# Performance work log

Measured on AMD Instinct MI355X. Metric: run time of the kernel, lower is better.

Reference implementation:

```python
import jax, jax.numpy as jnp
import numpy as np

NUM_UNITS = 512
NUM_IN = 256
BATCH = 8192


def _to_complex(x):
    # torch.view_as_complex on x.view(B, N, 2): even cols real, odd cols imag
    x2 = x.reshape(x.shape[0], -1, 2)
    return jax.lax.complex(x2[..., 0], x2[..., 1])


def _diag_mul(w, z):
    return (jnp.cos(w) + 1j * jnp.sin(w)) * z


def _reflect(re, im, z):
    v = jax.lax.complex(re, im)                      # [N]
    vstar_z = jnp.sum(jnp.conj(v) * z, axis=1, keepdims=True)  # [B,1]
    sq_norm = jnp.sum(re * re + im * im)
    return z - (2.0 / sq_norm) * vstar_z * v


def _modrelu(z, bias):
    norm = jnp.abs(z)
    scale = jax.nn.relu(norm + bias) / (norm + 1e-6)
    return scale * z


def setup_inputs() -> dict:
    key = jax.random.key(0)
    ks = jax.random.split(key, 12)
    two_pi = 2.0 * np.pi
    inputs = jax.random.normal(ks[0], (BATCH, NUM_IN), dtype=jnp.float32)
    states = jax.random.normal(ks[1], (BATCH, 2 * NUM_UNITS), dtype=jnp.float32)
    # xavier_uniform for w_ih [2N, num_in]
    bound = np.sqrt(6.0 / (2 * NUM_UNITS + NUM_IN)).astype(np.float32)
    w_ih = jax.random.uniform(ks[2], (2 * NUM_UNITS, NUM_IN), jnp.float32, -bound, bound)
    b_h = jnp.zeros((NUM_UNITS,), jnp.float32)
    d1_w = jax.random.uniform(ks[3], (NUM_UNITS,), jnp.float32, -np.pi, np.pi)
    d2_w = jax.random.uniform(ks[4], (NUM_UNITS,), jnp.float32, -np.pi, np.pi)
    d3_w = jax.random.uniform(ks[5], (NUM_UNITS,), jnp.float32, -np.pi, np.pi)
    r1_re = jax.random.uniform(ks[6], (NUM_UNITS,), jnp.float32, -1.0, 1.0)
    r1_im = jax.random.uniform(ks[7], (NUM_UNITS,), jnp.float32, -1.0, 1.0)
    r2_re = jax.random.uniform(ks[8], (NUM_UNITS,), jnp.float32, -1.0, 1.0)
    r2_im = jax.random.uniform(ks[9], (NUM_UNITS,), jnp.float32, -1.0, 1.0)
    perm = jax.random.permutation(ks[10], NUM_UNITS).astype(jnp.int64)
    return {"inputs": inputs, "states": states, "w_ih": w_ih, "b_h": b_h,
            "d1_w": d1_w, "r1_re": r1_re, "r1_im": r1_im, "perm": perm,
            "d2_w": d2_w, "r2_re": r2_re, "r2_im": r2_im, "d3_w": d3_w}


def reference(inputs, states, w_ih, b_h, d1_w, r1_re, r1_im, perm,
              d2_w, r2_re, r2_im, d3_w):
    inputs_mul = inputs @ w_ih.T                      # [B, 2N]
    inputs_mul_c = _to_complex(inputs_mul)            # [B, N] complex
    state_c = _to_complex(states)                     # [B, N] complex

    z = _diag_mul(d1_w, state_c)
    z = jnp.fft.fft(z, axis=1)
    z = _reflect(r1_re, r1_im, z)
    z = z[:, perm]
    z = _diag_mul(d2_w, z)
    z = jnp.fft.ifft(z, axis=1)
    z = _reflect(r2_re, r2_im, z)
    z = _diag_mul(d3_w, z)

    preact = inputs_mul_c + z
    new_c = _modrelu(preact, b_h)
    return jnp.concatenate([new_c.real, new_c.imag], axis=1)  # [B, 2N]
```

## Files before the change

kernel.cpp:

```cpp
#include <hip/hip_runtime.h>
#include <math.h>

#define BATCH 8192
#define NU 512
#define NIN 256

typedef __attribute__((ext_vector_type(8))) __bf16 bf16x8;
typedef __attribute__((ext_vector_type(4))) float f32x4;

__device__ __forceinline__ float2 cmul(float2 a, float2 b){
    return make_float2(a.x*b.x - a.y*b.y, a.x*b.y + a.y*b.x);
}
__device__ __forceinline__ float2 cadd(float2 a, float2 b){ return make_float2(a.x+b.x, a.y+b.y); }
__device__ __forceinline__ float2 csub(float2 a, float2 b){ return make_float2(a.x-b.x, a.y-b.y); }

__device__ __forceinline__ float2 cis_native(float ang){
    return make_float2(__cosf(ang), __sinf(ang));
}

template<bool INV>
__device__ __forceinline__ float2 twid512(int idx){
    float ang = 0.012271846303085129f * (float)idx;
    return cis_native(INV ? ang : -ang);
}

__device__ __forceinline__ unsigned int pack2bf(float x, float y){
    unsigned int ux = __float_as_uint(x);
    ux = (ux + 0x7FFFu + ((ux >> 16) & 1u)) >> 16;
    unsigned int uy = __float_as_uint(y);
    uy = (uy + 0x7FFFu + ((uy >> 16) & 1u)) & 0xFFFF0000u;
    return ux | uy;
}


__device__ __forceinline__ void stage_tile(const float* __restrict__ G,
                                           char* __restrict__ lds,
                                           int kb, int tid){
    const int r0 = tid >> 3;
    const int kc = (tid & 7) << 3;
    #pragma unroll
    for (int it = 0; it < 4; ++it){
        const int row = r0 + (it << 5);
        const float* g = G + (size_t)row * NIN + kb + kc;
        float4 v0 = *(const float4*)g;
        float4 v1 = *(const float4*)(g + 4);
        int4 w;
        w.x = (int)pack2bf(v0.x, v0.y);
        w.y = (int)pack2bf(v0.z, v0.w);
        w.z = (int)pack2bf(v1.x, v1.y);
        w.w = (int)pack2bf(v1.z, v1.w);
        int off = (row << 7) + (kc << 1);
        off ^= (row & 7) << 4;
        *(int4*)(lds + off) = w;
    }
}

__global__ __launch_bounds__(256) void gemm_bf16(const float* __restrict__ A,
                                                 const float* __restrict__ W,
                                                 float* __restrict__ P){
    __shared__ __align__(16) char smem[2 * 128*64*2];
    char* As = smem;
    char* Bs = smem + 128*64*2;
    const int tid  = threadIdx.x;
    const int lane = tid & 63, wv = tid >> 6;
    const int wm = wv >> 1, wn = wv & 1;
    const int bm = blockIdx.y, bn = blockIdx.x;

    const float* Ag = A + (size_t)bm * 128 * NIN;
    const float* Wg = W + (size_t)bn * 128 * NIN;

    f32x4 acc[4][4] = {};
    const int frow = lane & 15;
    const int kq   = (lane >> 4) << 4;

    for (int kb = 0; kb < NIN; kb += 64){
        if (kb) __syncthreads();
        stage_tile(Ag, As, kb, tid);
        stage_tile(Wg, Bs, kb, tid);
        __syncthreads();
        #pragma unroll
        for (int ks = 0; ks < 2; ++ks){
            const int koff = kq + (ks << 6);
            bf16x8 a[4], b[4];
            #pragma unroll
            for (int i = 0; i < 4; ++i){
                const int ar = wm*64 + i*16 + frow;
                a[i] = *(const bf16x8*)(As + (((ar << 7) + koff) ^ ((ar & 7) << 4)));
                const int br = wn*64 + i*16 + frow;
                b[i] = *(const bf16x8*)(Bs + (((br << 7) + koff) ^ ((br & 7) << 4)));
            }
            #pragma unroll
            for (int mi = 0; mi < 4; ++mi)
                #pragma unroll
                for (int ni = 0; ni < 4; ++ni)
                    acc[mi][ni] = __builtin_amdgcn_mfma_f32_16x16x32_bf16(
                        a[mi], b[ni], acc[mi][ni], 0, 0, 0);
        }
    }

    float* stg = (float*)smem;
    const int lr4 = (lane >> 4) << 2;
    #pragma unroll
    for (int q = 0; q < 4; ++q){
        __syncthreads();
        if (wm == (q >> 1)){
            const int miBase = (q & 1) * 2;
            #pragma unroll
            for (int mj = 0; mj < 2; ++mj)
                #pragma unroll
                for (int ni = 0; ni < 4; ++ni)
                    #pragma unroll
                    for (int r = 0; r < 4; ++r)
                        stg[(lr4 + mj*16 + r)*132 + wn*64 + ni*16 + frow]
                            = acc[miBase + mj][ni][r];
        }
        __syncthreads();
        #pragma unroll
        for (int it = 0; it < 4; ++it){
            int idx = it*256 + tid;
            int r32 = idx >> 5;
            int c4  = idx & 31;
            float4 v = *(const float4*)(stg + r32*132 + c4*4);
            int grow = bm*128 + (q >> 1)*64 + (q & 1)*32 + r32;
            *(float4*)(P + (size_t)grow*1024 + bn*128 + c4*4) = v;
        }
    }
}


__device__ __forceinline__ void fft_fwd(float2 z[8], int l){
    #pragma unroll
    for (int r = 0; r < 4; ++r){
        float2 w = twid512<false>(r*64 + l);
        float2 a = z[r], b = z[r+4];
        z[r]   = cadd(a, b);
        z[r+4] = cmul(w, csub(a, b));
    }
    {
        float2 w0 = twid512<false>(2*l), w1 = twid512<false>(2*(64+l));
        const int gs[4] = {0,1,4,5};
        #pragma unroll
        for (int k = 0; k < 4; ++k){
            int g = gs[k];
            float2 w = (g & 1) ? w1 : w0;
            float2 a = z[g], b = z[g+2];
            z[g]   = cadd(a, b);
            z[g+2] = cmul(w, csub(a, b));
        }
    }
    {
        float2 w = twid512<false>(4*l);
        #pragma unroll
        for (int g = 0; g < 8; g += 2){
            float2 a = z[g], b = z[g+1];
            z[g]   = cadd(a, b);
            z[g+1] = cmul(w, csub(a, b));
        }
    }
    #pragma unroll
    for (int h = 32; h >= 1; h >>= 1){
        int m = 256 / h;
        float2 w = twid512<false>(m * (l & (h-1)));
        bool low = (l & h) != 0;
        #pragma unroll
        for (int r = 0; r < 8; ++r){
            float2 p;
            p.x = __shfl_xor(z[r].x, h);
            p.y = __shfl_xor(z[r].y, h);
            z[r] = low ? cmul(w, csub(p, z[r])) : cadd(z[r], p);
        }
    }
}

__device__ __forceinline__ void fft_inv(float2 z[8], int l){
    #pragma unroll
    for (int h = 1; h <= 32; h <<= 1){
        int m = 256 / h;
        float2 w = twid512<true>(m * (l & (h-1)));
        bool low = (l & h) != 0;
        #pragma unroll
        for (int r = 0; r < 8; ++r){
            float2 p;
            p.x = __shfl_xor(z[r].x, h);
            p.y = __shfl_xor(z[r].y, h);
            float2 t = cmul(w, low ? z[r] : p);
            z[r] = low ? csub(p, t) : cadd(z[r], t);
        }
    }
    {
        float2 w = twid512<true>(4*l);
        #pragma unroll
        for (int g = 0; g < 8; g += 2){
            float2 b = cmul(w, z[g+1]);
            z[g+1] = csub(z[g], b);
            z[g]   = cadd(z[g], b);
        }
    }
    {
        float2 w0 = twid512<true>(2*l), w1 = twid512<true>(2*(64+l));
        const int gs[4] = {0,1,4,5};
        #pragma unroll
        for (int k = 0; k < 4; ++k){
            int g = gs[k];
            float2 w = (g & 1) ? w1 : w0;
            float2 b = cmul(w, z[g+2]);
            z[g+2] = csub(z[g], b);
            z[g]   = cadd(z[g], b);
        }
    }
    #pragma unroll
    for (int r = 0; r < 4; ++r){
        float2 w = twid512<true>(r*64 + l);
        float2 b = cmul(w, z[r+4]);
        z[r+4] = csub(z[r], b);
        z[r]   = cadd(z[r], b);
    }
}

__device__ __forceinline__ void wave_reflect(float2 z[8], const float2 v[8]){
    float pr = 0.f, pi = 0.f, nn = 0.f;
    #pragma unroll
    for (int r = 0; r < 8; ++r){
        pr += v[r].x*z[r].x + v[r].y*z[r].y;
        pi += v[r].x*z[r].y - v[r].y*z[r].x;
        nn += v[r].x*v[r].x + v[r].y*v[r].y;
    }
    #pragma unroll
    for (int off = 32; off > 0; off >>= 1){
        pr += __shfl_xor(pr, off);
        pi += __shfl_xor(pi, off);
        nn += __shfl_xor(nn, off);
    }
    float c2 = 2.0f / nn;
    float2 cc = make_float2(c2*pr, c2*pi);
    #pragma unroll
    for (int r = 0; r < 8; ++r)
        z[r] = csub(z[r], cmul(cc, v[r]));
}

__global__ __launch_bounds__(256, 8) void urnn_wave(
        const float* __restrict__ states,
        const float* __restrict__ b_h,
        const float* __restrict__ d1_w,
        const float* __restrict__ r1_re, const float* __restrict__ r1_im,
        const int* __restrict__ perm,
        const float* __restrict__ d2_w,
        const float* __restrict__ r2_re, const float* __restrict__ r2_im,
        const float* __restrict__ d3_w,
        float* __restrict__ out )
{
    __shared__ float2 zbuf[4][512];

    const int tid = threadIdx.x;
    const int l = tid & 63, wv = tid >> 6;

    const int row = blockIdx.x * 4 + wv;
    const float* srow = states + (size_t)row * 1024;
    float* orow = out + (size_t)row * 1024;

    float2 c[8];
    #pragma unroll
    for (int r = 0; r < 8; ++r) c[r] = ((const float2*)orow)[r*64 + l];

    float2 z[8];
    #pragma unroll
    for (int r = 0; r < 8; ++r){
        int e = r*64 + l;
        float2 st = ((const float2*)srow)[e];
        z[r] = cmul(cis_native(d1_w[e]), st);
    }

    fft_fwd(z, l);

    {
        float2 v[8];
        #pragma unroll
        for (int r = 0; r < 8; ++r){
            int i = __brev((unsigned)(r*64 + l)) >> 23;
            v[r] = make_float2(r1_re[i], r1_im[i]);
        }
        wave_reflect(z, v);
    }

    {
        float2* zw = zbuf[wv];
        #pragma unroll
        for (int r = 0; r < 8; ++r) zw[r*64 + l] = z[r];
        #pragma unroll
        for (int r = 0; r < 8; ++r){
            int s = r*64 + l;
            int i = __brev((unsigned)s) >> 23;
            int g = __brev((unsigned)perm[i]) >> 23;
            z[r] = cmul(cis_native(d2_w[i]), zw[g]);
        }
    }

    fft_inv(z, l);

    {
        float2 v[8];
        #pragma unroll
        for (int r = 0; r < 8; ++r){
            int e = r*64 + l;
            v[r] = make_float2(r2_re[e], r2_im[e]);
        }
        wave_reflect(z, v);
    }

    const float inv = 1.0f/512.0f;
    #pragma unroll
    for (int r = 0; r < 8; ++r){
        int e = r*64 + l;
        float2 zz = cmul(cis_native(d3_w[e]), z[r]);
        float2 pre = make_float2(c[r].x + zz.x*inv, c[r].y + zz.y*inv);
        float nrm = __builtin_amdgcn_sqrtf(pre.x*pre.x + pre.y*pre.y);
        float sc = fmaxf(nrm + b_h[e], 0.f) / (nrm + 1e-6f);
        orow[e]       = sc*pre.x;
        orow[e + 512] = sc*pre.y;
    }
}

extern "C" void kernel_launch(void* const* d_in, const int* in_sizes, int n_in,
                              void* d_out, int out_size, void* d_ws, size_t ws_size,
                              hipStream_t stream) {
    const float* inputs = (const float*)d_in[0];
    const float* states = (const float*)d_in[1];
    const float* w_ih   = (const float*)d_in[2];
    const float* b_h    = (const float*)d_in[3];
    const float* d1_w   = (const float*)d_in[4];
    const float* r1_re  = (const float*)d_in[5];
    const float* r1_im  = (const float*)d_in[6];
    const int*   perm   = (const int*)d_in[7];
    const float* d2_w   = (const float*)d_in[8];
    const float* r2_re  = (const float*)d_in[9];
    const float* r2_im  = (const float*)d_in[10];
    const float* d3_w   = (const float*)d_in[11];
    float* out = (float*)d_out;

    dim3 gA(8, 64);
    gemm_bf16<<<gA, 256, 0, stream>>>(inputs, w_ih, out);
    urnn_wave<<<BATCH/4, 256, 0, stream>>>(states, b_h, d1_w, r1_re, r1_im,
                                           perm, d2_w, r2_re, r2_im, d3_w, out);
}
```

Baseline: 180.8 us.

## Shrink GEMM tiles, pre-convert operands to bf16, process two rows per wave

The GEMM tile drops from 128x128 to 64x64, which gives four times as many blocks. When workspace is available, inputs and weights are first converted to bf16 by separate kernels so the GEMM loads packed bf16 directly. The FFT/uRNN kernel now processes two batch rows per wave, sharing twiddles, diagonal phases and reflection vectors, with occupancy bounds lowered to 4. This adds two extra launches and an extra bf16 round trip through global memory, and the two-row path raises register pressure.

```diff
diff --git a/kernel.cpp b/kernel.cpp
--- a/kernel.cpp
+++ b/kernel.cpp
@@ -17,7 +17,6 @@
 __device__ __forceinline__ float2 cis_native(float ang){
     return make_float2(__cosf(ang), __sinf(ang));
 }
-
 template<bool INV>
 __device__ __forceinline__ float2 twid512(int idx){
     float ang = 0.012271846303085129f * (float)idx;
@@ -32,67 +31,79 @@
     return ux | uy;
 }
 
-
-__device__ __forceinline__ void stage_tile(const float* __restrict__ G,
-                                           char* __restrict__ lds,
-                                           int kb, int tid){
-    const int r0 = tid >> 3;
-    const int kc = (tid & 7) << 3;
-    #pragma unroll
-    for (int it = 0; it < 4; ++it){
-        const int row = r0 + (it << 5);
-        const float* g = G + (size_t)row * NIN + kb + kc;
-        float4 v0 = *(const float4*)g;
-        float4 v1 = *(const float4*)(g + 4);
-        int4 w;
-        w.x = (int)pack2bf(v0.x, v0.y);
-        w.y = (int)pack2bf(v0.z, v0.w);
-        w.z = (int)pack2bf(v1.x, v1.y);
-        w.w = (int)pack2bf(v1.z, v1.w);
-        int off = (row << 7) + (kc << 1);
-        off ^= (row & 7) << 4;
-        *(int4*)(lds + off) = w;
-    }
-}
-
-__global__ __launch_bounds__(256) void gemm_bf16(const float* __restrict__ A,
-                                                 const float* __restrict__ W,
-                                                 float* __restrict__ P){
-    __shared__ __align__(16) char smem[2 * 128*64*2];
+__global__ __launch_bounds__(256) void cvt_bf16(const float4* __restrict__ src,
+                                                uint2* __restrict__ dst, int n4){
+    int i = blockIdx.x*256 + threadIdx.x;
+    if (i < n4){
+        float4 v = src[i];
+        dst[i] = make_uint2(pack2bf(v.x, v.y), pack2bf(v.z, v.w));
+    }
+}
+
+template<bool PRE>
+__global__ __launch_bounds__(256) void gemm64(const void* __restrict__ Asrc,
+                                              const void* __restrict__ Wsrc,
+                                              float* __restrict__ P){
+    __shared__ __align__(16) char smem[2*64*64*2];
     char* As = smem;
-    char* Bs = smem + 128*64*2;
+    char* Bs = smem + 8192;
     const int tid  = threadIdx.x;
     const int lane = tid & 63, wv = tid >> 6;
     const int wm = wv >> 1, wn = wv & 1;
     const int bm = blockIdx.y, bn = blockIdx.x;
-
-    const float* Ag = A + (size_t)bm * 128 * NIN;
-    const float* Wg = W + (size_t)bn * 128 * NIN;
-
-    f32x4 acc[4][4] = {};
+    const int sr = tid >> 2, qc = tid & 3;
+    const int ssw = (sr & 7) << 4;
+    const int soff = (sr << 7) + (qc << 5);
+
+    f32x4 acc[2][2] = {};
     const int frow = lane & 15;
     const int kq   = (lane >> 4) << 4;
 
     for (int kb = 0; kb < NIN; kb += 64){
         if (kb) __syncthreads();
-        stage_tile(Ag, As, kb, tid);
-        stage_tile(Wg, Bs, kb, tid);
+        if constexpr (PRE){
+            const int4* Ag = (const int4*)((const unsigned short*)Asrc + (size_t)(bm*64 + sr)*NIN + kb + qc*16);
+            const int4* Wg = (const int4*)((const unsigned short*)Wsrc + (size_t)(bn*64 + sr)*NIN + kb + qc*16);
+            *(int4*)(As + ( soff       ^ ssw)) = Ag[0];
+            *(int4*)(As + ((soff + 16) ^ ssw)) = Ag[1];
+            *(int4*)(Bs + ( soff       ^ ssw)) = Wg[0];
+            *(int4*)(Bs + ((soff + 16) ^ ssw)) = Wg[1];
+        } else {
+            const float* Ag = (const float*)Asrc + (size_t)(bm*64 + sr)*NIN + kb + qc*16;
+            const float* Wg = (const float*)Wsrc + (size_t)(bn*64 + sr)*NIN + kb + qc*16;
+            float4 a0 = *(const float4*)Ag,     a1 = *(const float4*)(Ag+4);
+            float4 a2 = *(const float4*)(Ag+8), a3 = *(const float4*)(Ag+12);
+            float4 w0 = *(const float4*)Wg,     w1 = *(const float4*)(Wg+4);
+            float4 w2 = *(const float4*)(Wg+8), w3 = *(const float4*)(Wg+12);
+            int4 pa0 = make_int4((int)pack2bf(a0.x,a0.y),(int)pack2bf(a0.z,a0.w),
+                                 (int)pack2bf(a1.x,a1.y),(int)pack2bf(a1.z,a1.w));
+            int4 pa1 = make_int4((int)pack2bf(a2.x,a2.y),(int)pack2bf(a2.z,a2.w),
+                                 (int)pack2bf(a3.x,a3.y),(int)pack2bf(a3.z,a3.w));
+            int4 pw0 = make_int4((int)pack2bf(w0.x,w0.y),(int)pack2bf(w0.z,w0.w),
+                                 (int)pack2bf(w1.x,w1.y),(int)pack2bf(w1.z,w1.w));
+            int4 pw1 = make_int4((int)pack2bf(w2.x,w2.y),(int)pack2bf(w2.z,w2.w),
+                                 (int)pack2bf(w3.x,w3.y),(int)pack2bf(w3.z,w3.w));
+            *(int4*)(As + ( soff       ^ ssw)) = pa0;
+            *(int4*)(As + ((soff + 16) ^ ssw)) = pa1;
+            *(int4*)(Bs + ( soff       ^ ssw)) = pw0;
+            *(int4*)(Bs + ((soff + 16) ^ ssw)) = pw1;
+        }
         __syncthreads();
         #pragma unroll
         for (int ks = 0; ks < 2; ++ks){
             const int koff = kq + (ks << 6);
-            bf16x8 a[4], b[4];
+            bf16x8 a[2], b[2];
             #pragma unroll
-            for (int i = 0; i < 4; ++i){
-                const int ar = wm*64 + i*16 + frow;
+            for (int i = 0; i < 2; ++i){
+                const int ar = wm*32 + i*16 + frow;
                 a[i] = *(const bf16x8*)(As + (((ar << 7) + koff) ^ ((ar & 7) << 4)));
-                const int br = wn*64 + i*16 + frow;
+                const int br = wn*32 + i*16 + frow;
                 b[i] = *(const bf16x8*)(Bs + (((br << 7) + koff) ^ ((br & 7) << 4)));
             }
             #pragma unroll
-            for (int mi = 0; mi < 4; ++mi)
+            for (int mi = 0; mi < 2; ++mi)
                 #pragma unroll
-                for (int ni = 0; ni < 4; ++ni)
+                for (int ni = 0; ni < 2; ++ni)
                     acc[mi][ni] = __builtin_amdgcn_mfma_f32_16x16x32_bf16(
                         a[mi], b[ni], acc[mi][ni], 0, 0, 0);
         }
@@ -101,40 +112,46 @@
     float* stg = (float*)smem;
     const int lr4 = (lane >> 4) << 2;
     #pragma unroll
-    for (int q = 0; q < 4; ++q){
+    for (int p = 0; p < 2; ++p){
         __syncthreads();
-        if (wm == (q >> 1)){
-            const int miBase = (q & 1) * 2;
+        if (wm == p){
             #pragma unroll
-            for (int mj = 0; mj < 2; ++mj)
+            for (int i = 0; i < 2; ++i)
                 #pragma unroll
-                for (int ni = 0; ni < 4; ++ni)
+                for (int j = 0; j < 2; ++j)
                     #pragma unroll
                     for (int r = 0; r < 4; ++r)
-                        stg[(lr4 + mj*16 + r)*132 + wn*64 + ni*16 + frow]
-                            = acc[miBase + mj][ni][r];
+                        stg[(i*16 + lr4 + r)*68 + wn*32 + j*16 + frow] = acc[i][j][r];
         }
         __syncthreads();
         #pragma unroll
-        for (int it = 0; it < 4; ++it){
+        for (int it = 0; it < 2; ++it){
             int idx = it*256 + tid;
-            int r32 = idx >> 5;
-            int c4  = idx & 31;
-            float4 v = *(const float4*)(stg + r32*132 + c4*4);
-            int grow = bm*128 + (q >> 1)*64 + (q & 1)*32 + r32;
-            *(float4*)(P + (size_t)grow*1024 + bn*128 + c4*4) = v;
-        }
-    }
-}
-
-
-__device__ __forceinline__ void fft_fwd(float2 z[8], int l){
+            int r32 = idx >> 4, c4 = idx & 15;
+            float4 v = *(const float4*)(stg + r32*68 + c4*4);
+            *(float4*)(P + (size_t)(bm*64 + p*32 + r32)*1024 + bn*64 + c4*4) = v;
+        }
+    }
+}
+
+
+__device__ __forceinline__ void bfly_f(float2& a, float2& b, float2 w){
+    float2 t = csub(a, b);
+    a = cadd(a, b);
+    b = cmul(w, t);
+}
+__device__ __forceinline__ void bfly_i(float2& a, float2& b, float2 w){
+    float2 t = cmul(w, b);
+    b = csub(a, t);
+    a = cadd(a, t);
+}
+
+__device__ __forceinline__ void fft_fwd2(float2 z0[8], float2 z1[8], int l){
     #pragma unroll
     for (int r = 0; r < 4; ++r){
         float2 w = twid512<false>(r*64 + l);
-        float2 a = z[r], b = z[r+4];
-        z[r]   = cadd(a, b);
-        z[r+4] = cmul(w, csub(a, b));
+        bfly_f(z0[r], z0[r+4], w);
+        bfly_f(z1[r], z1[r+4], w);
     }
     {
         float2 w0 = twid512<false>(2*l), w1 = twid512<false>(2*(64+l));
@@ -143,18 +160,16 @@
         for (int k = 0; k < 4; ++k){
             int g = gs[k];
             float2 w = (g & 1) ? w1 : w0;
-            float2 a = z[g], b = z[g+2];
-            z[g]   = cadd(a, b);
-            z[g+2] = cmul(w, csub(a, b));
+            bfly_f(z0[g], z0[g+2], w);
+            bfly_f(z1[g], z1[g+2], w);
         }
     }
     {
         float2 w = twid512<false>(4*l);
         #pragma unroll
         for (int g = 0; g < 8; g += 2){
-            float2 a = z[g], b = z[g+1];
-            z[g]   = cadd(a, b);
-            z[g+1] = cmul(w, csub(a, b));
+            bfly_f(z0[g], z0[g+1], w);
+            bfly_f(z1[g], z1[g+1], w);
         }
     }
     #pragma unroll
@@ -164,15 +179,18 @@
         bool low = (l & h) != 0;
         #pragma unroll
         for (int r = 0; r < 8; ++r){
-            float2 p;
-            p.x = __shfl_xor(z[r].x, h);
-            p.y = __shfl_xor(z[r].y, h);
-            z[r] = low ? cmul(w, csub(p, z[r])) : cadd(z[r], p);
-        }
-    }
-}
-
-__device__ __forceinline__ void fft_inv(float2 z[8], int l){
+            float2 p0, p1;
+            p0.x = __shfl_xor(z0[r].x, h);
+            p0.y = __shfl_xor(z0[r].y, h);
+            p1.x = __shfl_xor(z1[r].x, h);
+            p1.y = __shfl_xor(z1[r].y, h);
+            z0[r] = low ? cmul(w, csub(p0, z0[r])) : cadd(z0[r], p0);
+            z1[r] = low ? cmul(w, csub(p1, z1[r])) : cadd(z1[r], p1);
+        }
+    }
+}
+
+__device__ __forceinline__ void fft_inv2(float2 z0[8], float2 z1[8], int l){
     #pragma unroll
     for (int h = 1; h <= 32; h <<= 1){
         int m = 256 / h;
@@ -180,20 +198,23 @@
         bool low = (l & h) != 0;
         #pragma unroll
         for (int r = 0; r < 8; ++r){
-            float2 p;
-            p.x = __shfl_xor(z[r].x, h);
-            p.y = __shfl_xor(z[r].y, h);
-            float2 t = cmul(w, low ? z[r] : p);
-            z[r] = low ? csub(p, t) : cadd(z[r], t);
+            float2 p0, p1;
+            p0.x = __shfl_xor(z0[r].x, h);
+            p0.y = __shfl_xor(z0[r].y, h);
+            p1.x = __shfl_xor(z1[r].x, h);
+            p1.y = __shfl_xor(z1[r].y, h);
+            float2 t0 = cmul(w, low ? z0[r] : p0);
+            float2 t1 = cmul(w, low ? z1[r] : p1);
+            z0[r] = low ? csub(p0, t0) : cadd(z0[r], t0);
+            z1[r] = low ? csub(p1, t1) : cadd(z1[r], t1);
         }
     }
     {
         float2 w = twid512<true>(4*l);
         #pragma unroll
         for (int g = 0; g < 8; g += 2){
-            float2 b = cmul(w, z[g+1]);
-            z[g+1] = csub(z[g], b);
-            z[g]   = cadd(z[g], b);
+            bfly_i(z0[g], z0[g+1], w);
+            bfly_i(z1[g], z1[g+1], w);
         }
     }
     {
@@ -203,42 +224,48 @@
         for (int k = 0; k < 4; ++k){
             int g = gs[k];
             float2 w = (g & 1) ? w1 : w0;
-            float2 b = cmul(w, z[g+2]);
-            z[g+2] = csub(z[g], b);
-            z[g]   = cadd(z[g], b);
+            bfly_i(z0[g], z0[g+2], w);
+            bfly_i(z1[g], z1[g+2], w);
         }
     }
     #pragma unroll
     for (int r = 0; r < 4; ++r){
         float2 w = twid512<true>(r*64 + l);
-        float2 b = cmul(w, z[r+4]);
-        z[r+4] = csub(z[r], b);
-        z[r]   = cadd(z[r], b);
-    }
-}
-
-__device__ __forceinline__ void wave_reflect(float2 z[8], const float2 v[8]){
-    float pr = 0.f, pi = 0.f, nn = 0.f;
+        bfly_i(z0[r], z0[r+4], w);
+        bfly_i(z1[r], z1[r+4], w);
+    }
+}
+
+__device__ __forceinline__ void wave_reflect2(float2 z0[8], float2 z1[8],
+                                              const float2 v[8]){
+    float pr0=0.f, pi0=0.f, pr1=0.f, pi1=0.f, nn=0.f;
     #pragma unroll
     for (int r = 0; r < 8; ++r){
-        pr += v[r].x*z[r].x + v[r].y*z[r].y;
-        pi += v[r].x*z[r].y - v[r].y*z[r].x;
-        nn += v[r].x*v[r].x + v[r].y*v[r].y;
+        pr0 += v[r].x*z0[r].x + v[r].y*z0[r].y;
+        pi0 += v[r].x*z0[r].y - v[r].y*z0[r].x;
+        pr1 += v[r].x*z1[r].x + v[r].y*z1[r].y;
+        pi1 += v[r].x*z1[r].y - v[r].y*z1[r].x;
+        nn  += v[r].x*v[r].x + v[r].y*v[r].y;
     }
     #pragma unroll
     for (int off = 32; off > 0; off >>= 1){
-        pr += __shfl_xor(pr, off);
-        pi += __shfl_xor(pi, off);
-        nn += __shfl_xor(nn, off);
+        pr0 += __shfl_xor(pr0, off);
+        pi0 += __shfl_xor(pi0, off);
+        pr1 += __shfl_xor(pr1, off);
+        pi1 += __shfl_xor(pi1, off);
+        nn  += __shfl_xor(nn, off);
     }
     float c2 = 2.0f / nn;
-    float2 cc = make_float2(c2*pr, c2*pi);
-    #pragma unroll
-    for (int r = 0; r < 8; ++r)
-        z[r] = csub(z[r], cmul(cc, v[r]));
-}
-
-__global__ __launch_bounds__(256, 8) void urnn_wave(
+    float2 cc0 = make_float2(c2*pr0, c2*pi0);
+    float2 cc1 = make_float2(c2*pr1, c2*pi1);
+    #pragma unroll
+    for (int r = 0; r < 8; ++r){
+        z0[r] = csub(z0[r], cmul(cc0, v[r]));
+        z1[r] = csub(z1[r], cmul(cc1, v[r]));
+    }
+}
+
+__global__ __launch_bounds__(256, 4) void urnn_wave2(
         const float* __restrict__ states,
         const float* __restrict__ b_h,
         const float* __restrict__ d1_w,
@@ -249,28 +276,27 @@
         const float* __restrict__ d3_w,
         float* __restrict__ out )
 {
-    __shared__ float2 zbuf[4][512];
+    __shared__ float2 zbuf[4][2][512];
 
     const int tid = threadIdx.x;
     const int l = tid & 63, wv = tid >> 6;
 
-    const int row = blockIdx.x * 4 + wv;
-    const float* srow = states + (size_t)row * 1024;
-    float* orow = out + (size_t)row * 1024;
-
-    float2 c[8];
-    #pragma unroll
-    for (int r = 0; r < 8; ++r) c[r] = ((const float2*)orow)[r*64 + l];
-
-    float2 z[8];
+    const int rp = (blockIdx.x*4 + wv)*2;
+    const float* s0 = states + (size_t)rp * 1024;
+    const float* s1 = s0 + 1024;
+    float* o0 = out + (size_t)rp * 1024;
+    float* o1 = o0 + 1024;
+
+    float2 z0[8], z1[8];
     #pragma unroll
     for (int r = 0; r < 8; ++r){
         int e = r*64 + l;
-        float2 st = ((const float2*)srow)[e];
-        z[r] = cmul(cis_native(d1_w[e]), st);
-    }
-
-    fft_fwd(z, l);
+        float2 d = cis_native(d1_w[e]);
+        z0[r] = cmul(d, ((const float2*)s0)[e]);
+        z1[r] = cmul(d, ((const float2*)s1)[e]);
+    }
+
+    fft_fwd2(z0, z1, l);
 
     {
         float2 v[8];
@@ -279,23 +305,36 @@
             int i = __brev((unsigned)(r*64 + l)) >> 23;
             v[r] = make_float2(r1_re[i], r1_im[i]);
         }
-        wave_reflect(z, v);
-    }
-
-    {
-        float2* zw = zbuf[wv];
-        #pragma unroll
-        for (int r = 0; r < 8; ++r) zw[r*64 + l] = z[r];
+        wave_reflect2(z0, z1, v);
+    }
+
+    {
+        float2* zw0 = zbuf[wv][0];
+        float2* zw1 = zbuf[wv][1];
+        #pragma unroll
+        for (int r = 0; r < 8; ++r){
+            zw0[r*64 + l] = z0[r];
+            zw1[r*64 + l] = z1[r];
+        }
         #pragma unroll
         for (int r = 0; r < 8; ++r){
             int s = r*64 + l;
             int i = __brev((unsigned)s) >> 23;
             int g = __brev((unsigned)perm[i]) >> 23;
-            z[r] = cmul(cis_native(d2_w[i]), zw[g]);
-        }
-    }
-
-    fft_inv(z, l);
+            float2 d = cis_native(d2_w[i]);
+            z0[r] = cmul(d, zw0[g]);
+            z1[r] = cmul(d, zw1[g]);
+        }
+    }
+
+    fft_inv2(z0, z1, l);
+
+    float2 c0[8], c1[8];
+    #pragma unroll
+    for (int r = 0; r < 8; ++r){
+        c0[r] = ((const float2*)o0)[r*64 + l];
+        c1[r] = ((const float2*)o1)[r*64 + l];
+    }
 
     {
         float2 v[8];
@@ -304,19 +343,31 @@
             int e = r*64 + l;
             v[r] = make_float2(r2_re[e], r2_im[e]);
         }
-        wave_reflect(z, v);
+        wave_reflect2(z0, z1, v);
     }
 
     const float inv = 1.0f/512.0f;
     #pragma unroll
     for (int r = 0; r < 8; ++r){
         int e = r*64 + l;
-        float2 zz = cmul(cis_native(d3_w[e]), z[r]);
-        float2 pre = make_float2(c[r].x + zz.x*inv, c[r].y + zz.y*inv);
-        float nrm = __builtin_amdgcn_sqrtf(pre.x*pre.x + pre.y*pre.y);
-        float sc = fmaxf(nrm + b_h[e], 0.f) / (nrm + 1e-6f);
-        orow[e]       = sc*pre.x;
-        orow[e + 512] = sc*pre.y;
+        float2 d = cis_native(d3_w[e]);
+        float bh = b_h[e];
+        {
+            float2 zz = cmul(d, z0[r]);
+            float2 pre = make_float2(c0[r].x + zz.x*inv, c0[r].y + zz.y*inv);
+            float nrm = __builtin_amdgcn_sqrtf(pre.x*pre.x + pre.y*pre.y);
+            float sc = fmaxf(nrm + bh, 0.f) / (nrm + 1e-6f);
+            o0[e]       = sc*pre.x;
+            o0[e + 512] = sc*pre.y;
+        }
+        {
+            float2 zz = cmul(d, z1[r]);
+            float2 pre = make_float2(c1[r].x + zz.x*inv, c1[r].y + zz.y*inv);
+            float nrm = __builtin_amdgcn_sqrtf(pre.x*pre.x + pre.y*pre.y);
+            float sc = fmaxf(nrm + bh, 0.f) / (nrm + 1e-6f);
+            o1[e]       = sc*pre.x;
+            o1[e + 512] = sc*pre.y;
+        }
     }
 }
 
@@ -337,8 +388,21 @@
     const float* d3_w   = (const float*)d_in[11];
     float* out = (float*)d_out;
 
-    dim3 gA(8, 64);
-    gemm_bf16<<<gA, 256, 0, stream>>>(inputs, w_ih, out);
-    urnn_wave<<<BATCH/4, 256, 0, stream>>>(states, b_h, d1_w, r1_re, r1_im,
-                                           perm, d2_w, r2_re, r2_im, d3_w, out);
-}
+    const size_t needA = (size_t)BATCH * NIN * 2;
+    const size_t needW = (size_t)(2*NU) * NIN * 2;
+    dim3 gA(16, 128);
+
+    if (ws_size >= needA + needW){
+        unsigned short* Abf = (unsigned short*)d_ws;
+        unsigned short* Wbf = (unsigned short*)((char*)d_ws + needA);
+        cvt_bf16<<<(BATCH*NIN/4 + 255)/256, 256, 0, stream>>>(
+            (const float4*)inputs, (uint2*)Abf, BATCH*NIN/4);
+        cvt_bf16<<<(2*NU*NIN/4 + 255)/256, 256, 0, stream>>>(
+            (const float4*)w_ih, (uint2*)Wbf, 2*NU*NIN/4);
+        gemm64<true><<<gA, 256, 0, stream>>>(Abf, Wbf, out);
+    } else {
+        gemm64<false><<<gA, 256, 0, stream>>>(inputs, w_ih, out);
+    }
+    urnn_wave2<<<BATCH/8, 256, 0, stream>>>(states, b_h, d1_w, r1_re, r1_im,
+                                            perm, d2_w, r2_re, r2_im, d3_w, out);
+}
```

Measured after the change: 165.5 us. -8.4%, faster.
